# Performance work log

Measured on AMD Instinct MI355X. Metric: run time of the kernel, lower is better.

The kernel has to match this reference:

```python
import jax, jax.numpy as jnp
import numpy as np

D, NH, NL, NP, DFF = 256, 8, 4, 4, 1024
HD = D // NH
SHAPES = np.array([[100, 152], [50, 76], [25, 38], [13, 19]], dtype=np.int64)
LV = int((SHAPES[:, 0] * SHAPES[:, 1]).sum())  # 20197


def setup_inputs() -> dict:
    key = jax.random.key(0)
    ks = iter(jax.random.split(key, 48))
    bs, Lq = 8, 300

    def w(shape, s=0.02):
        return jax.random.normal(next(ks), shape, jnp.float32) * s

    lsi = np.concatenate([[0], np.cumsum(SHAPES[:, 0] * SHAPES[:, 1])[:-1]]).astype(np.int64)
    return dict(
        tgt=w((bs, Lq, D), 1.0),
        query_pos=w((bs, Lq, D), 1.0),
        reference_points=jax.random.uniform(next(ks), (bs, Lq, NL, 2), jnp.float32),
        src=w((bs, LV, D), 1.0),
        in_proj_w=w((3 * D, D)), in_proj_b=jnp.zeros((3 * D,), jnp.float32),
        out_proj_w=w((D, D)), out_proj_b=jnp.zeros((D,), jnp.float32),
        samp_off_w=w((NH * NL * NP * 2, D)), samp_off_b=w((NH * NL * NP * 2,), 0.5),
        attn_w_w=w((NH * NL * NP, D)), attn_w_b=jnp.zeros((NH * NL * NP,), jnp.float32),
        value_proj_w=w((D, D)), value_proj_b=jnp.zeros((D,), jnp.float32),
        output_proj_w=w((D, D)), output_proj_b=jnp.zeros((D,), jnp.float32),
        lin1_w=w((DFF, D)), lin1_b=jnp.zeros((DFF,), jnp.float32),
        lin2_w=w((D, DFF)), lin2_b=jnp.zeros((D,), jnp.float32),
        norm1_w=jnp.ones((D,), jnp.float32), norm1_b=jnp.zeros((D,), jnp.float32),
        norm2_w=jnp.ones((D,), jnp.float32), norm2_b=jnp.zeros((D,), jnp.float32),
        norm3_w=jnp.ones((D,), jnp.float32), norm3_b=jnp.zeros((D,), jnp.float32),
        spatial_shapes=SHAPES,            # static numpy (shapes must be static)
        level_start_index=lsi,            # static numpy
        padding_mask=jnp.zeros((bs, LV), bool),
    )


def _ln(x, w, b):
    m = x.mean(-1, keepdims=True)
    v = ((x - m) ** 2).mean(-1, keepdims=True)
    return (x - m) * jax.lax.rsqrt(v + 1e-5) * w + b


def _bilinear(vflat, H_, W_, loc):
    # vflat: (b,h,H*W,d); loc: (b,h,q,p,2) normalized to [0,1]
    # matches F.grid_sample(align_corners=False, padding_mode='zeros')
    x = loc[..., 0] * W_ - 0.5
    y = loc[..., 1] * H_ - 0.5
    x0f, y0f = jnp.floor(x), jnp.floor(y)
    lx, ly = x - x0f, y - y0f
    x0, y0 = x0f.astype(jnp.int32), y0f.astype(jnp.int32)
    b, h, q, p = x0.shape

    def gather(ix, iy, wgt):
        valid = (ix >= 0) & (ix < W_) & (iy >= 0) & (iy < H_)
        idx = (jnp.clip(iy, 0, H_ - 1) * W_ + jnp.clip(ix, 0, W_ - 1)).reshape(b, h, q * p)
        g = jnp.take_along_axis(vflat, idx[..., None], axis=2)  # (b,h,q*p,d)
        return g * (wgt * valid).reshape(b, h, q * p, 1)

    out = (gather(x0, y0, (1 - lx) * (1 - ly)) + gather(x0 + 1, y0, lx * (1 - ly))
           + gather(x0, y0 + 1, (1 - lx) * ly) + gather(x0 + 1, y0 + 1, lx * ly))
    return out.reshape(b, h, q, p, -1)


def reference(tgt, query_pos, reference_points, src, in_proj_w, in_proj_b,
              out_proj_w, out_proj_b, samp_off_w, samp_off_b, attn_w_w, attn_w_b,
              value_proj_w, value_proj_b, output_proj_w, output_proj_b,
              lin1_w, lin1_b, lin2_w, lin2_b, norm1_w, norm1_b, norm2_w, norm2_b,
              norm3_w, norm3_b, spatial_shapes, level_start_index, padding_mask):
    bs, Lq, _ = tgt.shape
    ss = np.asarray(spatial_shapes)
    lsi = np.asarray(level_start_index)

    # ---- self attention (eval mode, dropout off) ----
    qk = tgt + query_pos
    qh = (qk @ in_proj_w[:D].T + in_proj_b[:D]).reshape(bs, Lq, NH, HD)
    kh = (qk @ in_proj_w[D:2 * D].T + in_proj_b[D:2 * D]).reshape(bs, Lq, NH, HD)
    vh = (tgt @ in_proj_w[2 * D:].T + in_proj_b[2 * D:]).reshape(bs, Lq, NH, HD)
    scores = jnp.einsum('bqhd,bkhd->bhqk', qh, kh) / jnp.sqrt(jnp.float32(HD))
    attn = jax.nn.softmax(scores, axis=-1)
    sa = jnp.einsum('bhqk,bkhd->bqhd', attn, vh).reshape(bs, Lq, D)
    sa = sa @ out_proj_w.T + out_proj_b
    x = _ln(tgt + sa, norm2_w, norm2_b)

    # ---- MSDeformAttn cross attention ----
    query = x + query_pos
    value = src @ value_proj_w.T + value_proj_b
    value = jnp.where(padding_mask[..., None], 0.0, value)
    value_t = value.reshape(bs, -1, NH, HD).transpose(0, 2, 1, 3)  # (b,h,Lv,d)

    offsets = (query @ samp_off_w.T + samp_off_b).reshape(bs, Lq, NH, NL, NP, 2)
    aw = jax.nn.softmax((query @ attn_w_w.T + attn_w_b).reshape(bs, Lq, NH, NL * NP), -1)
    aw = aw.reshape(bs, Lq, NH, NL, NP)
    norma = jnp.asarray(np.stack([ss[:, 1], ss[:, 0]], -1), jnp.float32)  # (NL,2)=[W,H]
    loc = reference_points[:, :, None, :, None, :] + offsets / norma[None, None, None, :, None, :]

    out = jnp.zeros((bs, Lq, NH, HD), value.dtype)
    for l in range(NL):
        H_, W_ = int(ss[l, 0]), int(ss[l, 1])
        s0 = int(lsi[l])
        vl = value_t[:, :, s0:s0 + H_ * W_]                    # (b,h,HW,d)
        ll = loc[:, :, :, l].transpose(0, 2, 1, 3, 4)          # (b,h,q,p,2)
        samp = _bilinear(vl, H_, W_, ll)                       # (b,h,q,p,d)
        out = out + jnp.einsum('bhqpd,bqhp->bqhd', samp, aw[:, :, :, l])
    ca = out.reshape(bs, Lq, D) @ output_proj_w.T + output_proj_b
    x = _ln(x + ca, norm1_w, norm1_b)

    # ---- FFN ----
    ffn = jax.nn.relu(x @ lin1_w.T + lin1_b) @ lin2_w.T + lin2_b
    x = _ln(x + ffn, norm3_w, norm3_b)
    return (x, loc, aw)
```

## Files before the change

kernel.cpp:

```cpp
#include <hip/hip_runtime.h>
#include <hip/hip_bf16.h>

#define D_ 256
#define NH_ 8
#define HD_ 32
#define NL_ 4
#define NP_ 4
#define DFF_ 1024
#define BS_ 8
#define LQ_ 300
#define LV_ 20197
#define NQ_ (BS_*LQ_)
#define MPAD_ 2432
#define NSRC_ (BS_*LV_*D_)

typedef short bf16x8 __attribute__((ext_vector_type(8)));
typedef float f32x4  __attribute__((ext_vector_type(4)));

__device__ __forceinline__ float u2f(unsigned int u) {
    union { unsigned int i; float f; } v; v.i = u << 16; return v.f;
}
__device__ __forceinline__ float lo2f(unsigned int u) {
    union { unsigned int i; float f; } v; v.i = u << 16; return v.f;
}
__device__ __forceinline__ float hi2f(unsigned int u) {
    union { unsigned int i; float f; } v; v.i = u & 0xffff0000u; return v.f;
}
__device__ __forceinline__ unsigned short f2bf_bits(float f) {
    __hip_bfloat16 b = __float2bfloat16(f);
    union { __hip_bfloat16 b; unsigned short u; } v; v.b = b; return v.u;
}
__device__ __forceinline__ ushort4 cv4(float4 a) {
    ushort4 o; o.x=f2bf_bits(a.x); o.y=f2bf_bits(a.y); o.z=f2bf_bits(a.z); o.w=f2bf_bits(a.w);
    return o;
}

#define DOT4(accum, wv, ap) do { \
    float4 _a = *(const float4*)(ap); \
    accum += wv.x*_a.x + wv.y*_a.y + wv.z*_a.z + wv.w*_a.w; } while(0)

__global__ __launch_bounds__(256) void cvt_bf16_kernel(
    const float* __restrict__ src, unsigned short* __restrict__ vbf)
{
    const int nsrc4 = NSRC_/4;
    for (int i = blockIdx.x*256 + threadIdx.x; i < nsrc4; i += gridDim.x*256) {
        ((ushort4*)vbf)[i] = cv4(((const float4*)src)[i]);
    }
}

__global__ __launch_bounds__(256) void cvt_misc_kernel(
    const float4* __restrict__ tgt, const float4* __restrict__ qp,
    const float4* __restrict__ ipw, const float4* __restrict__ l1w,
    const float4* __restrict__ l2w,
    ushort4* __restrict__ tgt_bf, ushort4* __restrict__ qk_bf,
    ushort4* __restrict__ ipw_bf, ushort4* __restrict__ l1w_bf,
    ushort4* __restrict__ l2w_bf)
{
    const int i = blockIdx.x*256 + threadIdx.x;
    if (i < 153600) {
        float4 a = tgt[i], b = qp[i];
        tgt_bf[i] = cv4(a);
        qk_bf[i]  = cv4(make_float4(a.x+b.x, a.y+b.y, a.z+b.z, a.w+b.w));
    } else if (i < 202752) {
        int j = i - 153600; ipw_bf[j] = cv4(ipw[j]);
    } else if (i < 268288) {
        int j = i - 202752; l1w_bf[j] = cv4(l1w[j]);
    } else if (i < 333824) {
        int j = i - 268288; l2w_bf[j] = cv4(l2w[j]);
    }
}

__global__ __launch_bounds__(256) void pack_weights_kernel(
    const float4* __restrict__ ipw,  const float4* __restrict__ opw,
    const float4* __restrict__ sow,  const float4* __restrict__ aww,
    const float4* __restrict__ outw, const float4* __restrict__ l1w,
    const float4* __restrict__ l2w,  const float4* __restrict__ vpw,
    float4* __restrict__ ipwP,  float4* __restrict__ opwP,
    float4* __restrict__ sowP,  float4* __restrict__ awwP,
    float4* __restrict__ outwP, float4* __restrict__ l1wP,
    float4* __restrict__ l2wP,  float4* __restrict__ vpwP)
{
    __shared__ float4 tile[32][33];
    const int RS[8]  = {768,256,256,128,256,1024,256,256};
    const int C4S[8] = {64, 64, 64, 64, 64, 64, 256, 64};
    const int TCUM[9] = {0,48,64,80,88,104,168,232,248};
    int tb = blockIdx.x, mi = 0;
    while (tb >= TCUM[mi+1]) ++mi;
    const int lt = tb - TCUM[mi];
    const float4* in  = (mi==0)?ipw :(mi==1)?opw :(mi==2)?sow :(mi==3)?aww
                       :(mi==4)?outw:(mi==5)?l1w :(mi==6)?l2w :vpw;
    float4* out       = (mi==0)?ipwP:(mi==1)?opwP:(mi==2)?sowP:(mi==3)?awwP
                       :(mi==4)?outwP:(mi==5)?l1wP:(mi==6)?l2wP:vpwP;
    const int R = RS[mi], C4 = C4S[mi];
    const int tpr = C4 >> 5;
    const int by = lt / tpr, bx = lt % tpr;
    const int tx = threadIdx.x & 31, ty = threadIdx.x >> 5;
#pragma unroll
    for (int i = 0; i < 32; i += 8)
        tile[ty+i][tx] = in[(size_t)(by*32+ty+i)*C4 + bx*32+tx];
    __syncthreads();
#pragma unroll
    for (int i = 0; i < 32; i += 8)
        out[(size_t)(bx*32+ty+i)*R + by*32+tx] = tile[tx][ty+i];
}

__global__ __launch_bounds__(256) void gemm_bf16_kernel(
    const unsigned short* __restrict__ A,
    const unsigned short* __restrict__ W,
    const float* __restrict__ bias,
    float* __restrict__ out,
    unsigned short* __restrict__ out_bf,
    const int K, const int Nld, const int relu)
{
    const int t = threadIdx.x, wv = t >> 6, l = t & 63;
    const int m_base = blockIdx.x*64 + wv*16;
    const int n_base = blockIdx.y*64;
    const int lr = l & 15, lg = l >> 4;
    const unsigned short* ap = A + (size_t)(m_base + lr)*K + lg*8;
    const unsigned short* wp = W + (size_t)(n_base + lr)*K + lg*8;
    f32x4 ac0 = {0,0,0,0}, ac1 = {0,0,0,0}, ac2 = {0,0,0,0}, ac3 = {0,0,0,0};
    for (int k = 0; k < K; k += 32) {
        bf16x8 a  = *(const bf16x8*)(ap + k);
        bf16x8 b0 = *(const bf16x8*)(wp + k);
        bf16x8 b1 = *(const bf16x8*)(wp + (size_t)16*K + k);
        bf16x8 b2 = *(const bf16x8*)(wp + (size_t)32*K + k);
        bf16x8 b3 = *(const bf16x8*)(wp + (size_t)48*K + k);
        ac0 = __builtin_amdgcn_mfma_f32_16x16x32_bf16(a, b0, ac0, 0, 0, 0);
        ac1 = __builtin_amdgcn_mfma_f32_16x16x32_bf16(a, b1, ac1, 0, 0, 0);
        ac2 = __builtin_amdgcn_mfma_f32_16x16x32_bf16(a, b2, ac2, 0, 0, 0);
        ac3 = __builtin_amdgcn_mfma_f32_16x16x32_bf16(a, b3, ac3, 0, 0, 0);
    }
    const int orow0 = m_base + lg*4;
    const int ocol  = n_base + lr;
    const float b0v = bias[ocol], b1v = bias[ocol+16],
                b2v = bias[ocol+32], b3v = bias[ocol+48];
#pragma unroll
    for (int j = 0; j < 4; ++j) {
        const int row = orow0 + j;
        if (row < NQ_) {
            float v0 = ac0[j] + b0v, v1 = ac1[j] + b1v,
                  v2 = ac2[j] + b2v, v3 = ac3[j] + b3v;
            if (relu) {
                v0 = fmaxf(v0, 0.f); v1 = fmaxf(v1, 0.f);
                v2 = fmaxf(v2, 0.f); v3 = fmaxf(v3, 0.f);
            }
            const size_t base = (size_t)row*Nld + ocol;
            if (out) {
                out[base]    = v0; out[base+16] = v1;
                out[base+32] = v2; out[base+48] = v3;
            }
            if (out_bf) {
                out_bf[base]    = f2bf_bits(v0); out_bf[base+16] = f2bf_bits(v1);
                out_bf[base+32] = f2bf_bits(v2); out_bf[base+48] = f2bf_bits(v3);
            }
        }
    }
}

__global__ __launch_bounds__(256) void attn_kernel(
    const float* __restrict__ qh, const float* __restrict__ kh,
    const float* __restrict__ vh, float* __restrict__ sa)
{
    __shared__ unsigned short khl[LQ_][HD_+2];
    __shared__ unsigned short vhl[LQ_][HD_+2];
    __shared__ float sc[4][LQ_];
    __shared__ float qbuf[4][HD_];
    const int b = blockIdx.x >> 3, h = blockIdx.x & 7, chunk = blockIdx.y;
    const int t = threadIdx.x, w = t >> 6, lane = t & 63;
    for (int i = t; i < LQ_*HD_; i += 256) {
        int kq = i >> 5, d = i & 31;
        khl[kq][d] = f2bf_bits(kh[(b*LQ_ + kq)*D_ + h*HD_ + d]);
        vhl[kq][d] = f2bf_bits(vh[(b*LQ_ + kq)*D_ + h*HD_ + d]);
    }
    __syncthreads();
    const float scale = 0.17677669529663687f;
    for (int qi = 0; qi < 15; ++qi) {
        const int q = chunk*60 + w*15 + qi;
        if (lane < HD_) qbuf[w][lane] = qh[(b*LQ_ + q)*D_ + h*HD_ + lane];
        float qv[HD_];
#pragma unroll
        for (int d2 = 0; d2 < HD_; ++d2) qv[d2] = qbuf[w][d2];
        float mx = -1e30f;
        for (int k = lane; k < LQ_; k += 64) {
            float s = 0.f;
#pragma unroll
            for (int d2 = 0; d2 < HD_; ++d2) s += qv[d2]*u2f(khl[k][d2]);
            s *= scale;
            sc[w][k] = s;
            mx = fmaxf(mx, s);
        }
#pragma unroll
        for (int off = 32; off; off >>= 1) mx = fmaxf(mx, __shfl_xor(mx, off));
        float lsum = 0.f;
        for (int k = lane; k < LQ_; k += 64) {
            float e = __expf(sc[w][k] - mx);
            sc[w][k] = e; lsum += e;
        }
#pragma unroll
        for (int off = 32; off; off >>= 1) lsum += __shfl_xor(lsum, off);
        const int d = lane & 31, half = lane >> 5;
        float acc = 0.f;
        for (int k = half*150; k < half*150 + 150; ++k) acc += sc[w][k]*u2f(vhl[k][d]);
        acc += __shfl_down(acc, 32);
        if (lane < 32) sa[(b*LQ_ + q)*D_ + h*HD_ + d] = acc / lsum;
    }
}

__global__ __launch_bounds__(256) void proj_res_ln_kernel(
    const float* __restrict__ A, const float4* __restrict__ WP,
    const float* __restrict__ bias, const float* __restrict__ res,
    const float* __restrict__ gw, const float* __restrict__ gb,
    float* __restrict__ out, const float* __restrict__ qp,
    float* __restrict__ outq, unsigned short* __restrict__ out_bf)
{
    __shared__ float2 part[4][8];
    const int t = threadIdx.x, m0 = blockIdx.x * 8;
    const int w = t >> 6, lane = t & 63;
    const float* a0 = A + (size_t)m0*D_;
    float acc[8] = {0,0,0,0,0,0,0,0};
    const float4* w4 = WP + t;
#pragma unroll 4
    for (int c = 0; c < 64; ++c) {
        float4 wv = w4[c*256];
#pragma unroll
        for (int r = 0; r < 8; ++r) DOT4(acc[r], wv, a0 + r*D_ + c*4);
    }
    const float bb = bias[t], gwv = gw[t], gbv = gb[t];
    float v[8];
#pragma unroll
    for (int r = 0; r < 8; ++r) {
        v[r] = acc[r] + bb + res[(m0+r)*D_+t];
        float s = v[r], ss = v[r]*v[r];
#pragma unroll
        for (int off = 32; off; off >>= 1) {
            s += __shfl_xor(s, off); ss += __shfl_xor(ss, off);
        }
        if (lane == 0) part[w][r] = make_float2(s, ss);
    }
    __syncthreads();
#pragma unroll
    for (int r = 0; r < 8; ++r) {
        float2 p0 = part[0][r], p1 = part[1][r], p2 = part[2][r], p3 = part[3][r];
        float mean = (p0.x+p1.x+p2.x+p3.x) * (1.0f/256.0f);
        float ex2  = (p0.y+p1.y+p2.y+p3.y) * (1.0f/256.0f);
        float var  = ex2 - mean*mean;
        float o = (v[r]-mean) * rsqrtf(var + 1e-5f) * gwv + gbv;
        out[(m0+r)*D_+t] = o;
        if (outq)   outq[(m0+r)*D_+t] = o + qp[(m0+r)*D_+t];
        if (out_bf) out_bf[(m0+r)*D_+t] = f2bf_bits(o);
    }
}

__global__ __launch_bounds__(256) void res_ln_kernel(
    const float* __restrict__ y, const float* __restrict__ res,
    const float* __restrict__ gw, const float* __restrict__ gb,
    float* __restrict__ out)
{
    __shared__ float2 part[4][8];
    const int t = threadIdx.x, m0 = blockIdx.x * 8;
    const int w = t >> 6, lane = t & 63;
    const float gwv = gw[t], gbv = gb[t];
    float v[8];
#pragma unroll
    for (int r = 0; r < 8; ++r) {
        v[r] = y[(m0+r)*D_+t] + res[(m0+r)*D_+t];
        float s = v[r], ss = v[r]*v[r];
#pragma unroll
        for (int off = 32; off; off >>= 1) {
            s += __shfl_xor(s, off); ss += __shfl_xor(ss, off);
        }
        if (lane == 0) part[w][r] = make_float2(s, ss);
    }
    __syncthreads();
#pragma unroll
    for (int r = 0; r < 8; ++r) {
        float2 p0 = part[0][r], p1 = part[1][r], p2 = part[2][r], p3 = part[3][r];
        float mean = (p0.x+p1.x+p2.x+p3.x) * (1.0f/256.0f);
        float ex2  = (p0.y+p1.y+p2.y+p3.y) * (1.0f/256.0f);
        float var  = ex2 - mean*mean;
        out[(m0+r)*D_+t] = (v[r]-mean) * rsqrtf(var + 1e-5f) * gwv + gbv;
    }
}

__global__ __launch_bounds__(256) void samp_params_kernel(
    const float* __restrict__ x1q,
    const float4* __restrict__ sowP, const float* __restrict__ so_b,
    const float4* __restrict__ awwP, const float* __restrict__ aw_b,
    const float* __restrict__ refp,
    float* __restrict__ loc_out, float* __restrict__ aw_out)
{
    __shared__ float logits[8][128];
    const int t = threadIdx.x, m0 = blockIdx.x * 8;
    const float* a0 = x1q + (size_t)m0*D_;
    {
        float acc[8] = {0,0,0,0,0,0,0,0};
        const float4* w4 = sowP + t;
#pragma unroll 4
        for (int c = 0; c < 64; ++c) {
            float4 wv = w4[c*256];
#pragma unroll
            for (int r = 0; r < 8; ++r) DOT4(acc[r], wv, a0 + r*D_ + c*4);
        }
        const float ob = so_b[t];
        const int c_ = t & 1, l_ = (t >> 3) & 3;
        float nrm;
        if (c_ == 0) nrm = (l_==0)?152.f:(l_==1)?76.f:(l_==2)?38.f:19.f;
        else         nrm = (l_==0)?100.f:(l_==1)?50.f:(l_==2)?25.f:13.f;
        for (int r = 0; r < 8; ++r) {
            int m = m0 + r;
            float off = acc[r] + ob;
            loc_out[m*256 + t] = refp[(m*NL_ + l_)*2 + c_] + off / nrm;
        }
    }
    if (t < 128) {
        float acc[8] = {0,0,0,0,0,0,0,0};
        const float4* w4 = awwP + t;
#pragma unroll 4
        for (int c = 0; c < 64; ++c) {
            float4 wv = w4[c*128];
#pragma unroll
            for (int r = 0; r < 8; ++r) DOT4(acc[r], wv, a0 + r*D_ + c*4);
        }
        const float ab = aw_b[t];
        for (int r = 0; r < 8; ++r) logits[r][t] = acc[r] + ab;
    }
    __syncthreads();
    if (t < 128) {
        const int g0 = (t >> 4) << 4;
        for (int r = 0; r < 8; ++r) {
            float mx = -1e30f;
            for (int j = 0; j < 16; ++j) mx = fmaxf(mx, logits[r][g0+j]);
            float s = 0.f;
            for (int j = 0; j < 16; ++j) s += __expf(logits[r][g0+j] - mx);
            aw_out[(m0+r)*128 + t] = __expf(logits[r][t] - mx) / s;
        }
    }
}

__global__ __launch_bounds__(256) void samp_fuse_bf16_kernel(
    const unsigned short* __restrict__ vbf,
    const float* __restrict__ loc_f, const float* __restrict__ aw_f,
    float* __restrict__ svec_g, float* __restrict__ wsum_g)
{
    __shared__ int   cidx[128][4];
    __shared__ float cwt[128][4];
    const int m = blockIdx.x, t = threadIdx.x;
    const int b = m / LQ_;

    if (t < 128) {
        const int l = (t >> 2) & 3;
        const int HS[4] = {100,50,25,13}, WS[4] = {152,76,38,19}, S0[4] = {0,15200,19000,19950};
        const int Hh = HS[l], Ww = WS[l], s0 = S0[l];
        const float aw = aw_f[m*128 + t];
        const float x = loc_f[m*256 + 2*t]*Ww - 0.5f;
        const float y = loc_f[m*256 + 2*t + 1]*Hh - 0.5f;
        const float x0f = floorf(x), y0f = floorf(y);
        const int x0 = (int)x0f, y0 = (int)y0f;
        const float fx = x - x0f, fy = y - y0f;
        const int   cx[4] = {x0, x0+1, x0,   x0+1};
        const int   cy[4] = {y0, y0,   y0+1, y0+1};
        const float cw[4] = {(1.f-fx)*(1.f-fy), fx*(1.f-fy), (1.f-fx)*fy, fx*fy};
        float sw = 0.f;
#pragma unroll
        for (int j = 0; j < 4; ++j) {
            const bool valid = (cx[j] >= 0) & (cx[j] < Ww) & (cy[j] >= 0) & (cy[j] < Hh);
            cidx[t][j] = valid ? (s0 + cy[j]*Ww + cx[j]) : s0;
            float wv = valid ? aw*cw[j] : 0.f;
            cwt[t][j] = wv;
            sw += wv;
        }
#pragma unroll
        for (int off = 8; off; off >>= 1) sw += __shfl_xor(sw, off);
        if ((t & 15) == 0) wsum_g[m*NH_ + (t >> 4)] = sw;
    }
    __syncthreads();

    const int hh = (t >> 7) * 4;
    const int c  = t & 127;
    const unsigned int* sb = (const unsigned int*)(vbf + (size_t)b*LV_*D_) + c;
#pragma unroll
    for (int h = hh; h < hh + 4; ++h) {
        float e0=0.f, e1=0.f, e2=0.f, e3=0.f;
        float o0=0.f, o1=0.f, o2=0.f, o3=0.f;
#pragma unroll 4
        for (int s = 0; s < 16; ++s) {
            const int base = h*16 + s;
            const int   i0 = cidx[base][0], i1 = cidx[base][1],
                        i2 = cidx[base][2], i3 = cidx[base][3];
            const float w0 = cwt[base][0], w1 = cwt[base][1],
                        w2 = cwt[base][2], w3 = cwt[base][3];
            const unsigned int u0 = sb[(size_t)i0*128];
            const unsigned int u1 = sb[(size_t)i1*128];
            const unsigned int u2 = sb[(size_t)i2*128];
            const unsigned int u3 = sb[(size_t)i3*128];
            e0 += w0*lo2f(u0); o0 += w0*hi2f(u0);
            e1 += w1*lo2f(u1); o1 += w1*hi2f(u1);
            e2 += w2*lo2f(u2); o2 += w2*hi2f(u2);
            e3 += w3*lo2f(u3); o3 += w3*hi2f(u3);
        }
        *(float2*)&svec_g[(size_t)m*(NH_*D_) + h*D_ + 2*c] =
            make_float2((e0+e1)+(e2+e3), (o0+o1)+(o2+o3));
    }
}

__global__ __launch_bounds__(256) void vproj_kernel(
    const float* __restrict__ svec_g, const float* __restrict__ wsum_g,
    const float4* __restrict__ vpwP, const float* __restrict__ vpb,
    float* __restrict__ vo)
{
    __shared__ float sv[4][NH_*D_];
    const int t = threadIdx.x, m0 = blockIdx.x * 4;
    for (int i = t; i < 4*NH_*D_; i += 256)
        sv[i >> 11][i & 2047] = svec_g[(size_t)m0*(NH_*D_) + i];
    __syncthreads();
    const int h = t >> 5;
    const float4* w4 = vpwP + t;
    float a0 = 0.f, a1 = 0.f, a2 = 0.f, a3 = 0.f;
    for (int c = 0; c < 64; ++c) {
        const float4 wq = w4[c*256];
        const float4 s0 = *(const float4*)&sv[0][h*D_ + c*4];
        const float4 s1 = *(const float4*)&sv[1][h*D_ + c*4];
        const float4 s2 = *(const float4*)&sv[2][h*D_ + c*4];
        const float4 s3 = *(const float4*)&sv[3][h*D_ + c*4];
        a0 += wq.x*s0.x + wq.y*s0.y + wq.z*s0.z + wq.w*s0.w;
        a1 += wq.x*s1.x + wq.y*s1.y + wq.z*s1.z + wq.w*s1.w;
        a2 += wq.x*s2.x + wq.y*s2.y + wq.z*s2.z + wq.w*s2.w;
        a3 += wq.x*s3.x + wq.y*s3.y + wq.z*s3.z + wq.w*s3.w;
    }
    const float bb = vpb[t];
    vo[(size_t)(m0+0)*D_ + t] = a0 + bb*wsum_g[(m0+0)*NH_ + h];
    vo[(size_t)(m0+1)*D_ + t] = a1 + bb*wsum_g[(m0+1)*NH_ + h];
    vo[(size_t)(m0+2)*D_ + t] = a2 + bb*wsum_g[(m0+2)*NH_ + h];
    vo[(size_t)(m0+3)*D_ + t] = a3 + bb*wsum_g[(m0+3)*NH_ + h];
}

extern "C" void kernel_launch(void* const* d_in, const int* in_sizes, int n_in,
                              void* d_out, int out_size, void* d_ws, size_t ws_size,
                              hipStream_t stream) {
    (void)in_sizes; (void)n_in; (void)out_size; (void)ws_size;
    const float* tgt  = (const float*)d_in[0];
    const float* qpos = (const float*)d_in[1];
    const float* refp = (const float*)d_in[2];
    const float* srcp = (const float*)d_in[3];
    const float* ipw  = (const float*)d_in[4];
    const float* ipb  = (const float*)d_in[5];
    const float* opw  = (const float*)d_in[6];
    const float* opb  = (const float*)d_in[7];
    const float* sow  = (const float*)d_in[8];
    const float* sob  = (const float*)d_in[9];
    const float* aww  = (const float*)d_in[10];
    const float* awb  = (const float*)d_in[11];
    const float* vpw  = (const float*)d_in[12];
    const float* vpb  = (const float*)d_in[13];
    const float* outw = (const float*)d_in[14];
    const float* outb = (const float*)d_in[15];
    const float* l1w  = (const float*)d_in[16];
    const float* l1b  = (const float*)d_in[17];
    const float* l2w  = (const float*)d_in[18];
    const float* l2b  = (const float*)d_in[19];
    const float* n1w  = (const float*)d_in[20];
    const float* n1b  = (const float*)d_in[21];
    const float* n2w  = (const float*)d_in[22];
    const float* n2b  = (const float*)d_in[23];
    const float* n3w  = (const float*)d_in[24];
    const float* n3b  = (const float*)d_in[25];

    float* wsf = (float*)d_ws;
    float* qh   = wsf;
    float* kh   = wsf + 614400;
    float* vh   = wsf + 1228800;
    float* sa   = wsf + 1843200;
    float* x1   = wsf + 2457600;
    float* vo   = wsf + 3072000;
    float* x2   = wsf + 3686400;
    float* y3   = wsf + 4300800;
    float* x1q  = wsf + 4915200;
    float* P0   = wsf + 5529600;
    float4* ipwP  = (float4*)(P0);
    float4* opwP  = (float4*)(P0 + 196608);
    float4* sowP  = (float4*)(P0 + 262144);
    float4* awwP  = (float4*)(P0 + 327680);
    float4* outwP = (float4*)(P0 + 360448);
    float4* l1wP  = (float4*)(P0 + 425984);
    float4* l2wP  = (float4*)(P0 + 688128);
    float4* vpwP  = (float4*)(P0 + 950272);
    unsigned short* hid_bf = (unsigned short*)(wsf + 6545408);
    unsigned short* tgt_bf = (unsigned short*)(wsf + 7790592);
    unsigned short* qk_bf  = (unsigned short*)(wsf + 8101888);
    unsigned short* x2_bf  = (unsigned short*)(wsf + 8413184);
    unsigned short* ipw_bf = (unsigned short*)(wsf + 8724480);
    unsigned short* l1w_bf = (unsigned short*)(wsf + 8822784);
    unsigned short* l2w_bf = (unsigned short*)(wsf + 8953856);
    unsigned short* vbf    = (unsigned short*)(wsf + 9084928);
    float* svec_g = wsf + 9084928 + 20681728;
    float* wsum_g = svec_g + 4915200;

    float* xout   = (float*)d_out;
    float* locout = xout + 614400;
    float* awout  = xout + 1228800;

    pack_weights_kernel<<<248, 256, 0, stream>>>(
        (const float4*)ipw, (const float4*)opw, (const float4*)sow,
        (const float4*)aww, (const float4*)outw, (const float4*)l1w,
        (const float4*)l2w, (const float4*)vpw,
        ipwP, opwP, sowP, awwP, outwP, l1wP, l2wP, vpwP);
    cvt_misc_kernel<<<1304, 256, 0, stream>>>(
        (const float4*)tgt, (const float4*)qpos, (const float4*)ipw,
        (const float4*)l1w, (const float4*)l2w,
        (ushort4*)tgt_bf, (ushort4*)qk_bf, (ushort4*)ipw_bf,
        (ushort4*)l1w_bf, (ushort4*)l2w_bf);
    cvt_bf16_kernel<<<2048, 256, 0, stream>>>(srcp, vbf);

    gemm_bf16_kernel<<<dim3(38, 4), 256, 0, stream>>>(qk_bf,  ipw_bf,          ipb,       qh, nullptr, 256, 256, 0);
    gemm_bf16_kernel<<<dim3(38, 4), 256, 0, stream>>>(qk_bf,  ipw_bf + 65536,  ipb + 256, kh, nullptr, 256, 256, 0);
    gemm_bf16_kernel<<<dim3(38, 4), 256, 0, stream>>>(tgt_bf, ipw_bf + 131072, ipb + 512, vh, nullptr, 256, 256, 0);

    attn_kernel<<<dim3(BS_*NH_, 5), 256, 0, stream>>>(qh, kh, vh, sa);
    proj_res_ln_kernel<<<NQ_/8, 256, 0, stream>>>(sa, opwP, opb, tgt, n2w, n2b,
                                                  x1, qpos, x1q, nullptr);
    samp_params_kernel<<<NQ_/8, 256, 0, stream>>>(x1q, sowP, sob, awwP, awb, refp,
                                                  locout, awout);
    samp_fuse_bf16_kernel<<<NQ_, 256, 0, stream>>>(vbf, locout, awout, svec_g, wsum_g);
    vproj_kernel<<<NQ_/4, 256, 0, stream>>>(svec_g, wsum_g, vpwP, vpb, vo);
    proj_res_ln_kernel<<<NQ_/8, 256, 0, stream>>>(vo, outwP, outb, x1, n1w, n1b,
                                                  x2, nullptr, nullptr, x2_bf);
    gemm_bf16_kernel<<<dim3(38, 16), 256, 0, stream>>>(x2_bf,  l1w_bf, l1b, nullptr, hid_bf, 256, 1024, 1);
    gemm_bf16_kernel<<<dim3(38, 4),  256, 0, stream>>>(hid_bf, l2w_bf, l2b, y3, nullptr, 1024, 256, 0);
    res_ln_kernel<<<NQ_/8, 256, 0, stream>>>(y3, x2, n3w, n3b, xout);
}
```

Measured before the change: 592.2 us.

## Route output, sampling-offset and attention-weight projections through bf16 MFMA GEMM

```diff
diff --git a/kernel.cpp b/kernel.cpp
--- a/kernel.cpp
+++ b/kernel.cpp
@@ -35,10 +35,6 @@
     return o;
 }
 
-#define DOT4(accum, wv, ap) do { \
-    float4 _a = *(const float4*)(ap); \
-    accum += wv.x*_a.x + wv.y*_a.y + wv.z*_a.z + wv.w*_a.w; } while(0)
-
 __global__ __launch_bounds__(256) void cvt_bf16_kernel(
     const float* __restrict__ src, unsigned short* __restrict__ vbf)
 {
@@ -51,57 +47,43 @@
 __global__ __launch_bounds__(256) void cvt_misc_kernel(
     const float4* __restrict__ tgt, const float4* __restrict__ qp,
     const float4* __restrict__ ipw, const float4* __restrict__ l1w,
-    const float4* __restrict__ l2w,
+    const float4* __restrict__ l2w, const float4* __restrict__ opw,
+    const float4* __restrict__ outw, const float4* __restrict__ sow,
+    const float4* __restrict__ aww,
     ushort4* __restrict__ tgt_bf, ushort4* __restrict__ qk_bf,
     ushort4* __restrict__ ipw_bf, ushort4* __restrict__ l1w_bf,
-    ushort4* __restrict__ l2w_bf)
+    ushort4* __restrict__ l2w_bf, ushort4* __restrict__ opw_bf,
+    ushort4* __restrict__ outw_bf, ushort4* __restrict__ sow_bf,
+    ushort4* __restrict__ aww_bf)
 {
     const int i = blockIdx.x*256 + threadIdx.x;
     if (i < 153600) {
         float4 a = tgt[i], b = qp[i];
         tgt_bf[i] = cv4(a);
         qk_bf[i]  = cv4(make_float4(a.x+b.x, a.y+b.y, a.z+b.z, a.w+b.w));
-    } else if (i < 202752) {
-        int j = i - 153600; ipw_bf[j] = cv4(ipw[j]);
-    } else if (i < 268288) {
-        int j = i - 202752; l1w_bf[j] = cv4(l1w[j]);
-    } else if (i < 333824) {
-        int j = i - 268288; l2w_bf[j] = cv4(l2w[j]);
-    }
-}
-
-__global__ __launch_bounds__(256) void pack_weights_kernel(
-    const float4* __restrict__ ipw,  const float4* __restrict__ opw,
-    const float4* __restrict__ sow,  const float4* __restrict__ aww,
-    const float4* __restrict__ outw, const float4* __restrict__ l1w,
-    const float4* __restrict__ l2w,  const float4* __restrict__ vpw,
-    float4* __restrict__ ipwP,  float4* __restrict__ opwP,
-    float4* __restrict__ sowP,  float4* __restrict__ awwP,
-    float4* __restrict__ outwP, float4* __restrict__ l1wP,
-    float4* __restrict__ l2wP,  float4* __restrict__ vpwP)
+    } else if (i < 202752) { int j = i - 153600; ipw_bf[j]  = cv4(ipw[j]);
+    } else if (i < 268288) { int j = i - 202752; l1w_bf[j]  = cv4(l1w[j]);
+    } else if (i < 333824) { int j = i - 268288; l2w_bf[j]  = cv4(l2w[j]);
+    } else if (i < 350208) { int j = i - 333824; opw_bf[j]  = cv4(opw[j]);
+    } else if (i < 366592) { int j = i - 350208; outw_bf[j] = cv4(outw[j]);
+    } else if (i < 382976) { int j = i - 366592; sow_bf[j]  = cv4(sow[j]);
+    } else if (i < 391168) { int j = i - 382976; aww_bf[j]  = cv4(aww[j]);
+    }
+}
+
+__global__ __launch_bounds__(256) void pack_vpw_kernel(
+    const float4* __restrict__ vpw, float4* __restrict__ vpwP)
 {
     __shared__ float4 tile[32][33];
-    const int RS[8]  = {768,256,256,128,256,1024,256,256};
-    const int C4S[8] = {64, 64, 64, 64, 64, 64, 256, 64};
-    const int TCUM[9] = {0,48,64,80,88,104,168,232,248};
-    int tb = blockIdx.x, mi = 0;
-    while (tb >= TCUM[mi+1]) ++mi;
-    const int lt = tb - TCUM[mi];
-    const float4* in  = (mi==0)?ipw :(mi==1)?opw :(mi==2)?sow :(mi==3)?aww
-                       :(mi==4)?outw:(mi==5)?l1w :(mi==6)?l2w :vpw;
-    float4* out       = (mi==0)?ipwP:(mi==1)?opwP:(mi==2)?sowP:(mi==3)?awwP
-                       :(mi==4)?outwP:(mi==5)?l1wP:(mi==6)?l2wP:vpwP;
-    const int R = RS[mi], C4 = C4S[mi];
-    const int tpr = C4 >> 5;
-    const int by = lt / tpr, bx = lt % tpr;
+    const int by = blockIdx.x >> 1, bx = blockIdx.x & 1;
     const int tx = threadIdx.x & 31, ty = threadIdx.x >> 5;
 #pragma unroll
     for (int i = 0; i < 32; i += 8)
-        tile[ty+i][tx] = in[(size_t)(by*32+ty+i)*C4 + bx*32+tx];
+        tile[ty+i][tx] = vpw[(size_t)(by*32+ty+i)*64 + bx*32+tx];
     __syncthreads();
 #pragma unroll
     for (int i = 0; i < 32; i += 8)
-        out[(size_t)(bx*32+ty+i)*R + by*32+tx] = tile[tx][ty+i];
+        vpwP[(size_t)(bx*32+ty+i)*256 + by*32+tx] = tile[tx][ty+i];
 }
 
 __global__ __launch_bounds__(256) void gemm_bf16_kernel(
@@ -159,7 +141,7 @@
 
 __global__ __launch_bounds__(256) void attn_kernel(
     const float* __restrict__ qh, const float* __restrict__ kh,
-    const float* __restrict__ vh, float* __restrict__ sa)
+    const float* __restrict__ vh, unsigned short* __restrict__ sa_bf)
 {
     __shared__ unsigned short khl[LQ_][HD_+2];
     __shared__ unsigned short vhl[LQ_][HD_+2];
@@ -202,34 +184,24 @@
         float acc = 0.f;
         for (int k = half*150; k < half*150 + 150; ++k) acc += sc[w][k]*u2f(vhl[k][d]);
         acc += __shfl_down(acc, 32);
-        if (lane < 32) sa[(b*LQ_ + q)*D_ + h*HD_ + d] = acc / lsum;
-    }
-}
-
-__global__ __launch_bounds__(256) void proj_res_ln_kernel(
-    const float* __restrict__ A, const float4* __restrict__ WP,
-    const float* __restrict__ bias, const float* __restrict__ res,
+        if (lane < 32) sa_bf[(size_t)(b*LQ_ + q)*D_ + h*HD_ + d] = f2bf_bits(acc / lsum);
+    }
+}
+
+__global__ __launch_bounds__(256) void res_ln_kernel(
+    const float* __restrict__ y, const float* __restrict__ res,
     const float* __restrict__ gw, const float* __restrict__ gb,
     float* __restrict__ out, const float* __restrict__ qp,
-    float* __restrict__ outq, unsigned short* __restrict__ out_bf)
+    unsigned short* __restrict__ outq_bf, unsigned short* __restrict__ out_bf)
 {
     __shared__ float2 part[4][8];
     const int t = threadIdx.x, m0 = blockIdx.x * 8;
     const int w = t >> 6, lane = t & 63;
-    const float* a0 = A + (size_t)m0*D_;
-    float acc[8] = {0,0,0,0,0,0,0,0};
-    const float4* w4 = WP + t;
-#pragma unroll 4
-    for (int c = 0; c < 64; ++c) {
-        float4 wv = w4[c*256];
-#pragma unroll
-        for (int r = 0; r < 8; ++r) DOT4(acc[r], wv, a0 + r*D_ + c*4);
-    }
-    const float bb = bias[t], gwv = gw[t], gbv = gb[t];
+    const float gwv = gw[t], gbv = gb[t];
     float v[8];
 #pragma unroll
     for (int r = 0; r < 8; ++r) {
-        v[r] = acc[r] + bb + res[(m0+r)*D_+t];
+        v[r] = y[(m0+r)*D_+t] + res[(m0+r)*D_+t];
         float s = v[r], ss = v[r]*v[r];
 #pragma unroll
         for (int off = 32; off; off >>= 1) {
@@ -246,93 +218,37 @@
         float var  = ex2 - mean*mean;
         float o = (v[r]-mean) * rsqrtf(var + 1e-5f) * gwv + gbv;
         out[(m0+r)*D_+t] = o;
-        if (outq)   outq[(m0+r)*D_+t] = o + qp[(m0+r)*D_+t];
-        if (out_bf) out_bf[(m0+r)*D_+t] = f2bf_bits(o);
-    }
-}
-
-__global__ __launch_bounds__(256) void res_ln_kernel(
-    const float* __restrict__ y, const float* __restrict__ res,
-    const float* __restrict__ gw, const float* __restrict__ gb,
-    float* __restrict__ out)
-{
-    __shared__ float2 part[4][8];
-    const int t = threadIdx.x, m0 = blockIdx.x * 8;
-    const int w = t >> 6, lane = t & 63;
-    const float gwv = gw[t], gbv = gb[t];
-    float v[8];
-#pragma unroll
-    for (int r = 0; r < 8; ++r) {
-        v[r] = y[(m0+r)*D_+t] + res[(m0+r)*D_+t];
-        float s = v[r], ss = v[r]*v[r];
-#pragma unroll
-        for (int off = 32; off; off >>= 1) {
-            s += __shfl_xor(s, off); ss += __shfl_xor(ss, off);
-        }
-        if (lane == 0) part[w][r] = make_float2(s, ss);
-    }
-    __syncthreads();
-#pragma unroll
-    for (int r = 0; r < 8; ++r) {
-        float2 p0 = part[0][r], p1 = part[1][r], p2 = part[2][r], p3 = part[3][r];
-        float mean = (p0.x+p1.x+p2.x+p3.x) * (1.0f/256.0f);
-        float ex2  = (p0.y+p1.y+p2.y+p3.y) * (1.0f/256.0f);
-        float var  = ex2 - mean*mean;
-        out[(m0+r)*D_+t] = (v[r]-mean) * rsqrtf(var + 1e-5f) * gwv + gbv;
-    }
-}
-
-__global__ __launch_bounds__(256) void samp_params_kernel(
-    const float* __restrict__ x1q,
-    const float4* __restrict__ sowP, const float* __restrict__ so_b,
-    const float4* __restrict__ awwP, const float* __restrict__ aw_b,
+        if (outq_bf) outq_bf[(m0+r)*D_+t] = f2bf_bits(o + qp[(m0+r)*D_+t]);
+        if (out_bf)  out_bf[(m0+r)*D_+t]  = f2bf_bits(o);
+    }
+}
+
+__global__ __launch_bounds__(256) void samp_epi_kernel(
+    const float* __restrict__ so, const float* __restrict__ awl,
     const float* __restrict__ refp,
     float* __restrict__ loc_out, float* __restrict__ aw_out)
 {
-    __shared__ float logits[8][128];
+    __shared__ float lg[8][128];
     const int t = threadIdx.x, m0 = blockIdx.x * 8;
-    const float* a0 = x1q + (size_t)m0*D_;
-    {
-        float acc[8] = {0,0,0,0,0,0,0,0};
-        const float4* w4 = sowP + t;
-#pragma unroll 4
-        for (int c = 0; c < 64; ++c) {
-            float4 wv = w4[c*256];
-#pragma unroll
-            for (int r = 0; r < 8; ++r) DOT4(acc[r], wv, a0 + r*D_ + c*4);
-        }
-        const float ob = so_b[t];
-        const int c_ = t & 1, l_ = (t >> 3) & 3;
-        float nrm;
-        if (c_ == 0) nrm = (l_==0)?152.f:(l_==1)?76.f:(l_==2)?38.f:19.f;
-        else         nrm = (l_==0)?100.f:(l_==1)?50.f:(l_==2)?25.f:13.f;
-        for (int r = 0; r < 8; ++r) {
-            int m = m0 + r;
-            float off = acc[r] + ob;
-            loc_out[m*256 + t] = refp[(m*NL_ + l_)*2 + c_] + off / nrm;
-        }
-    }
-    if (t < 128) {
-        float acc[8] = {0,0,0,0,0,0,0,0};
-        const float4* w4 = awwP + t;
-#pragma unroll 4
-        for (int c = 0; c < 64; ++c) {
-            float4 wv = w4[c*128];
-#pragma unroll
-            for (int r = 0; r < 8; ++r) DOT4(acc[r], wv, a0 + r*D_ + c*4);
-        }
-        const float ab = aw_b[t];
-        for (int r = 0; r < 8; ++r) logits[r][t] = acc[r] + ab;
-    }
-    __syncthreads();
+    for (int i = t; i < 8*128; i += 256) lg[i >> 7][i & 127] = awl[m0*128 + i];
+    __syncthreads();
+    const int c_ = t & 1, l_ = (t >> 3) & 3;
+    float nrm;
+    if (c_ == 0) nrm = (l_==0)?152.f:(l_==1)?76.f:(l_==2)?38.f:19.f;
+    else         nrm = (l_==0)?100.f:(l_==1)?50.f:(l_==2)?25.f:13.f;
+#pragma unroll
+    for (int r = 0; r < 8; ++r) {
+        const int m = m0 + r;
+        loc_out[m*256 + t] = refp[(m*NL_ + l_)*2 + c_] + so[m*256 + t] / nrm;
+    }
     if (t < 128) {
         const int g0 = (t >> 4) << 4;
         for (int r = 0; r < 8; ++r) {
             float mx = -1e30f;
-            for (int j = 0; j < 16; ++j) mx = fmaxf(mx, logits[r][g0+j]);
+            for (int j = 0; j < 16; ++j) mx = fmaxf(mx, lg[r][g0+j]);
             float s = 0.f;
-            for (int j = 0; j < 16; ++j) s += __expf(logits[r][g0+j] - mx);
-            aw_out[(m0+r)*128 + t] = __expf(logits[r][t] - mx) / s;
+            for (int j = 0; j < 16; ++j) s += __expf(lg[r][g0+j] - mx);
+            aw_out[(m0+r)*128 + t] = __expf(lg[r][t] - mx) / s;
         }
     }
 }
@@ -406,7 +322,7 @@
 __global__ __launch_bounds__(256) void vproj_kernel(
     const float* __restrict__ svec_g, const float* __restrict__ wsum_g,
     const float4* __restrict__ vpwP, const float* __restrict__ vpb,
-    float* __restrict__ vo)
+    unsigned short* __restrict__ vo_bf)
 {
     __shared__ float sv[4][NH_*D_];
     const int t = threadIdx.x, m0 = blockIdx.x * 4;
@@ -428,10 +344,10 @@
         a3 += wq.x*s3.x + wq.y*s3.y + wq.z*s3.z + wq.w*s3.w;
     }
     const float bb = vpb[t];
-    vo[(size_t)(m0+0)*D_ + t] = a0 + bb*wsum_g[(m0+0)*NH_ + h];
-    vo[(size_t)(m0+1)*D_ + t] = a1 + bb*wsum_g[(m0+1)*NH_ + h];
-    vo[(size_t)(m0+2)*D_ + t] = a2 + bb*wsum_g[(m0+2)*NH_ + h];
-    vo[(size_t)(m0+3)*D_ + t] = a3 + bb*wsum_g[(m0+3)*NH_ + h];
+    vo_bf[(size_t)(m0+0)*D_ + t] = f2bf_bits(a0 + bb*wsum_g[(m0+0)*NH_ + h]);
+    vo_bf[(size_t)(m0+1)*D_ + t] = f2bf_bits(a1 + bb*wsum_g[(m0+1)*NH_ + h]);
+    vo_bf[(size_t)(m0+2)*D_ + t] = f2bf_bits(a2 + bb*wsum_g[(m0+2)*NH_ + h]);
+    vo_bf[(size_t)(m0+3)*D_ + t] = f2bf_bits(a3 + bb*wsum_g[(m0+3)*NH_ + h]);
 }
 
 extern "C" void kernel_launch(void* const* d_in, const int* in_sizes, int n_in,
@@ -469,62 +385,64 @@
     float* qh   = wsf;
     float* kh   = wsf + 614400;
     float* vh   = wsf + 1228800;
-    float* sa   = wsf + 1843200;
-    float* x1   = wsf + 2457600;
-    float* vo   = wsf + 3072000;
-    float* x2   = wsf + 3686400;
-    float* y3   = wsf + 4300800;
-    float* x1q  = wsf + 4915200;
-    float* P0   = wsf + 5529600;
-    float4* ipwP  = (float4*)(P0);
-    float4* opwP  = (float4*)(P0 + 196608);
-    float4* sowP  = (float4*)(P0 + 262144);
-    float4* awwP  = (float4*)(P0 + 327680);
-    float4* outwP = (float4*)(P0 + 360448);
-    float4* l1wP  = (float4*)(P0 + 425984);
-    float4* l2wP  = (float4*)(P0 + 688128);
-    float4* vpwP  = (float4*)(P0 + 950272);
-    unsigned short* hid_bf = (unsigned short*)(wsf + 6545408);
-    unsigned short* tgt_bf = (unsigned short*)(wsf + 7790592);
-    unsigned short* qk_bf  = (unsigned short*)(wsf + 8101888);
-    unsigned short* x2_bf  = (unsigned short*)(wsf + 8413184);
-    unsigned short* ipw_bf = (unsigned short*)(wsf + 8724480);
-    unsigned short* l1w_bf = (unsigned short*)(wsf + 8822784);
-    unsigned short* l2w_bf = (unsigned short*)(wsf + 8953856);
-    unsigned short* vbf    = (unsigned short*)(wsf + 9084928);
-    float* svec_g = wsf + 9084928 + 20681728;
+    float* x1   = wsf + 1843200;
+    float* x2   = wsf + 2457600;
+    float* y    = wsf + 3072000;
+    float* so_o = wsf + 3686400;
+    float* awl  = wsf + 4300800;
+    unsigned short* hid_bf  = (unsigned short*)(wsf + 4608000);
+    unsigned short* tgt_bf  = (unsigned short*)(wsf + 5853184);
+    unsigned short* qk_bf   = (unsigned short*)(wsf + 6164480);
+    unsigned short* sa_bf   = (unsigned short*)(wsf + 6475776);
+    unsigned short* x1q_bf  = (unsigned short*)(wsf + 6787072);
+    unsigned short* vo_bf   = (unsigned short*)(wsf + 7098368);
+    unsigned short* x2_bf   = (unsigned short*)(wsf + 7409664);
+    unsigned short* ipw_bf  = (unsigned short*)(wsf + 7720960);
+    unsigned short* l1w_bf  = (unsigned short*)(wsf + 7819264);
+    unsigned short* l2w_bf  = (unsigned short*)(wsf + 7950336);
+    unsigned short* opw_bf  = (unsigned short*)(wsf + 8081408);
+    unsigned short* outw_bf = (unsigned short*)(wsf + 8114176);
+    unsigned short* sow_bf  = (unsigned short*)(wsf + 8146944);
+    unsigned short* aww_bf  = (unsigned short*)(wsf + 8179712);
+    float4* vpwP = (float4*)(wsf + 8196096);
+    unsigned short* vbf = (unsigned short*)(wsf + 8261632);
+    float* svec_g = wsf + 8261632 + 20681728;
     float* wsum_g = svec_g + 4915200;
 
     float* xout   = (float*)d_out;
     float* locout = xout + 614400;
     float* awout  = xout + 1228800;
 
-    pack_weights_kernel<<<248, 256, 0, stream>>>(
-        (const float4*)ipw, (const float4*)opw, (const float4*)sow,
-        (const float4*)aww, (const float4*)outw, (const float4*)l1w,
-        (const float4*)l2w, (const float4*)vpw,
-        ipwP, opwP, sowP, awwP, outwP, l1wP, l2wP, vpwP);
-    cvt_misc_kernel<<<1304, 256, 0, stream>>>(
+    cvt_misc_kernel<<<1528, 256, 0, stream>>>(
         (const float4*)tgt, (const float4*)qpos, (const float4*)ipw,
-        (const float4*)l1w, (const float4*)l2w,
+        (const float4*)l1w, (const float4*)l2w, (const float4*)opw,
+        (const float4*)outw, (const float4*)sow, (const float4*)aww,
         (ushort4*)tgt_bf, (ushort4*)qk_bf, (ushort4*)ipw_bf,
-        (ushort4*)l1w_bf, (ushort4*)l2w_bf);
+        (ushort4*)l1w_bf, (ushort4*)l2w_bf, (ushort4*)opw_bf,
+        (ushort4*)outw_bf, (ushort4*)sow_bf, (ushort4*)aww_bf);
+    pack_vpw_kernel<<<16, 256, 0, stream>>>((const float4*)vpw, vpwP);
     cvt_bf16_kernel<<<2048, 256, 0, stream>>>(srcp, vbf);
 
     gemm_bf16_kernel<<<dim3(38, 4), 256, 0, stream>>>(qk_bf,  ipw_bf,          ipb,       qh, nullptr, 256, 256, 0);
     gemm_bf16_kernel<<<dim3(38, 4), 256, 0, stream>>>(qk_bf,  ipw_bf + 65536,  ipb + 256, kh, nullptr, 256, 256, 0);
     gemm_bf16_kernel<<<dim3(38, 4), 256, 0, stream>>>(tgt_bf, ipw_bf + 131072, ipb + 512, vh, nullptr, 256, 256, 0);
 
-    attn_kernel<<<dim3(BS_*NH_, 5), 256, 0, stream>>>(qh, kh, vh, sa);
-    proj_res_ln_kernel<<<NQ_/8, 256, 0, stream>>>(sa, opwP, opb, tgt, n2w, n2b,
-                                                  x1, qpos, x1q, nullptr);
-    samp_params_kernel<<<NQ_/8, 256, 0, stream>>>(x1q, sowP, sob, awwP, awb, refp,
-                                                  locout, awout);
+    attn_kernel<<<dim3(BS_*NH_, 5), 256, 0, stream>>>(qh, kh, vh, sa_bf);
+
+    gemm_bf16_kernel<<<dim3(38, 4), 256, 0, stream>>>(sa_bf, opw_bf, opb, y, nullptr, 256, 256, 0);
+    res_ln_kernel<<<NQ_/8, 256, 0, stream>>>(y, tgt, n2w, n2b, x1, qpos, x1q_bf, nullptr);
+
+    gemm_bf16_kernel<<<dim3(38, 4), 256, 0, stream>>>(x1q_bf, sow_bf, sob, so_o, nullptr, 256, 256, 0);
+    gemm_bf16_kernel<<<dim3(38, 2), 256, 0, stream>>>(x1q_bf, aww_bf, awb, awl, nullptr, 256, 128, 0);
+    samp_epi_kernel<<<NQ_/8, 256, 0, stream>>>(so_o, awl, refp, locout, awout);
+
     samp_fuse_bf16_kernel<<<NQ_, 256, 0, stream>>>(vbf, locout, awout, svec_g, wsum_g);
-    vproj_kernel<<<NQ_/4, 256, 0, stream>>>(svec_g, wsum_g, vpwP, vpb, vo);
-    proj_res_ln_kernel<<<NQ_/8, 256, 0, stream>>>(vo, outwP, outb, x1, n1w, n1b,
-                                                  x2, nullptr, nullptr, x2_bf);
+    vproj_kernel<<<NQ_/4, 256, 0, stream>>>(svec_g, wsum_g, vpwP, vpb, vo_bf);
+
+    gemm_bf16_kernel<<<dim3(38, 4), 256, 0, stream>>>(vo_bf, outw_bf, outb, y, nullptr, 256, 256, 0);
+    res_ln_kernel<<<NQ_/8, 256, 0, stream>>>(y, x1, n1w, n1b, x2, nullptr, nullptr, x2_bf);
+
     gemm_bf16_kernel<<<dim3(38, 16), 256, 0, stream>>>(x2_bf,  l1w_bf, l1b, nullptr, hid_bf, 256, 1024, 1);
-    gemm_bf16_kernel<<<dim3(38, 4),  256, 0, stream>>>(hid_bf, l2w_bf, l2b, y3, nullptr, 1024, 256, 0);
-    res_ln_kernel<<<NQ_/8, 256, 0, stream>>>(y3, x2, n3w, n3b, xout);
-}
+    gemm_bf16_kernel<<<dim3(38, 4),  256, 0, stream>>>(hid_bf, l2w_bf, l2b, y, nullptr, 1024, 256, 0);
+    res_ln_kernel<<<NQ_/8, 256, 0, stream>>>(y, x2, n3w, n3b, xout, nullptr, nullptr, nullptr);
+}
```

Result: faster. 550.9 us (-7.0%).
